# Kernel tuning notes

Measured on AMD Instinct MI355X. Metric: run time of the kernel, lower is better.

## Reference

```python
import jax, jax.numpy as jnp
import numpy as np

N = 8192      # nb_nodes
HID = 128     # hid_dim
OUT = 64      # out_dim
E = 262144    # num edges (avg degree 32)
BN_EPS = 1e-5


def setup_inputs() -> dict:
    key = jax.random.key(0)
    ks = jax.random.split(key, 10)
    x = jax.random.normal(ks[0], (N, HID), dtype=jnp.float32)
    adj = jnp.zeros((N, N), dtype=jnp.float32)  # unused by the module's forward
    src = jax.random.randint(ks[1], (E,), 0, N)
    dst = jax.random.randint(ks[2], (E,), 0, N)
    s = 0.05
    fc_w = jax.random.normal(ks[3], (HID, OUT), dtype=jnp.float32) * s
    fc_b = jnp.zeros((OUT,), dtype=jnp.float32)
    w1 = jax.random.normal(ks[4], (HID, HID), dtype=jnp.float32) * s
    w1_b = jnp.zeros((HID,), dtype=jnp.float32)
    w2 = jax.random.normal(ks[5], (HID, OUT), dtype=jnp.float32) * s
    w2_b = jnp.zeros((OUT,), dtype=jnp.float32)
    epsilon = jnp.full((N,), 0.5, dtype=jnp.float32)  # init.constant_(0.5)
    gamma = jnp.ones((OUT,), dtype=jnp.float32)
    beta = jnp.zeros((OUT,), dtype=jnp.float32)
    return {"x": x, "adj": adj, "src": src, "dst": dst,
            "fc_w": fc_w, "fc_b": fc_b, "w1": w1, "w1_b": w1_b,
            "w2": w2, "w2_b": w2_b, "epsilon": epsilon,
            "gamma": gamma, "beta": beta}


def _neighbor_sum(feat, src, dst):
    # DGL copy_src + sum: each dst node sums features of its src neighbors.
    return jax.ops.segment_sum(feat[src], dst, num_segments=N)


def reference(x, adj, src, dst, fc_w, fc_b, w1, w1_b, w2, w2_b, epsilon, gamma, beta):
    # h1 = fc(x)
    h1 = x @ fc_w + fc_b                                  # [N, OUT]
    # layer1: neighbor-sum then linear, ReLU
    h2 = jax.nn.relu(_neighbor_sum(x, src, dst) @ w1 + w1_b)   # [N, HID]
    # layer2: neighbor-sum then linear
    h2 = _neighbor_sum(h2, src, dst) @ w2 + w2_b          # [N, OUT]
    eps = epsilon[:, None]
    h = (1.0 - eps) * h1 + eps * h2                       # [N, OUT]
    ret = (h @ h.T + x @ x.T) * 0.5                       # [N, N]
    # BatchNorm1d (training mode: batch stats, biased variance)
    mean = jnp.mean(h, axis=0)
    var = jnp.var(h, axis=0)
    h_bn = (h - mean) * jax.lax.rsqrt(var + BN_EPS) * gamma + beta
    return ret, h_bn
```

## Files before the change

kernel.cpp:

```cpp
#include <hip/hip_runtime.h>
#include <hip/hip_bf16.h>

#define N_NODES 8192
#define HID 128
#define OUT_F 64
#define E_EDGES 262144
#define KTOT 192

typedef __bf16 bf16x8 __attribute__((ext_vector_type(8)));
typedef float  f32x4  __attribute__((ext_vector_type(4)));

__device__ __forceinline__ unsigned short f2bf(float f) {
    unsigned int u = __float_as_uint(f);
    u += 0x7fffu + ((u >> 16) & 1u);
    return (unsigned short)(u >> 16);
}

__global__ void count_k(const int* __restrict__ dst, int* __restrict__ cnt) {
    int e = blockIdx.x * 256 + threadIdx.x;
    if (e < E_EDGES) atomicAdd(&cnt[dst[e]], 1);
}

__global__ void scan_k(const int* __restrict__ cnt, int* __restrict__ off,
                       int* __restrict__ cursor, float* __restrict__ stats) {
    __shared__ int part[256];
    int tid = threadIdx.x;
    if (tid < 128) stats[tid] = 0.0f;
    int base = tid * 32;
    int local[32];
    int s = 0;
    #pragma unroll
    for (int j = 0; j < 32; ++j) { local[j] = s; s += cnt[base + j]; }
    part[tid] = s;
    __syncthreads();
    if (tid == 0) {
        int acc = 0;
        for (int i = 0; i < 256; ++i) { int t = part[i]; part[i] = acc; acc += t; }
    }
    __syncthreads();
    int p = part[tid];
    #pragma unroll
    for (int j = 0; j < 32; ++j) {
        int v = p + local[j];
        off[base + j] = v;
        cursor[base + j] = v;
    }
    if (tid == 255) off[N_NODES] = p + s;
}

__global__ void fill_k(const int* __restrict__ src, const int* __restrict__ dst,
                       int* __restrict__ cursor, int* __restrict__ eidx) {
    int e = blockIdx.x * 256 + threadIdx.x;
    if (e >= E_EDGES) return;
    int pos = atomicAdd(&cursor[dst[e]], 1);
    eidx[pos] = src[e];
}

__global__ __launch_bounds__(256)
void pre_k(const float* __restrict__ x,
           const float* __restrict__ fcw, const float* __restrict__ fcb,
           const float* __restrict__ w1,
           float* __restrict__ h1, float* __restrict__ y,
           unsigned short* __restrict__ G) {
    __shared__ float wS[64 * 192];
    __shared__ float xs[16 * HID];
    int tid = threadIdx.x;
    int rowbase = blockIdx.x * 16;

    for (int i = tid; i < 512; i += 256)
        *(float4*)&xs[i * 4] = *(const float4*)&x[(size_t)rowbase * HID + i * 4];

    int c = tid & 63, r0 = tid >> 6;
    float acc[3][4] = {};

    for (int kh = 0; kh < 2; ++kh) {
        __syncthreads();
        for (int i = tid; i < 1024; i += 256) {
            int k = i >> 4, qd = i & 15;
            *(float4*)&wS[k * 192 + qd * 4] =
                *(const float4*)&fcw[(size_t)(kh * 64 + k) * 64 + qd * 4];
        }
        for (int i = tid; i < 2048; i += 256) {
            int k = i >> 5, qd = i & 31;
            *(float4*)&wS[k * 192 + 64 + qd * 4] =
                *(const float4*)&w1[(size_t)(kh * 64 + k) * 128 + qd * 4];
        }
        __syncthreads();
        #pragma unroll 4
        for (int k = 0; k < 64; ++k) {
            float wa = wS[k * 192 + c];
            float wb = wS[k * 192 + 64 + c];
            float wc = wS[k * 192 + 128 + c];
            #pragma unroll
            for (int g = 0; g < 4; ++g) {
                float xv = xs[(r0 + 4 * g) * HID + kh * 64 + k];
                acc[0][g] += xv * wa;
                acc[1][g] += xv * wb;
                acc[2][g] += xv * wc;
            }
        }
    }
    float b = fcb[c];
    #pragma unroll
    for (int g = 0; g < 4; ++g) {
        int r = rowbase + r0 + 4 * g;
        h1[(size_t)r * OUT_F + c]    = acc[0][g] + b;
        y[(size_t)r * HID + c]       = acc[1][g];
        y[(size_t)r * HID + 64 + c]  = acc[2][g];
    }
    const float SC = 0.70710678f;
    for (int i = tid; i < 2048; i += 256) {
        int r = i >> 7, cc = i & 127;
        G[(size_t)(rowbase + r) * KTOT + OUT_F + cc] = f2bf(xs[r * HID + cc] * SC);
    }
}

__global__ __launch_bounds__(256)
void gather_mlp_k(const float* __restrict__ feat,
                  const int* __restrict__ eidx,
                  const int* __restrict__ off,
                  const float* __restrict__ bias,
                  const float* __restrict__ w2,
                  float* __restrict__ z) {
    __shared__ float wS[HID * 64];
    __shared__ float rowS[4][HID];
    int tid = threadIdx.x;
    int wid = tid >> 6, lane = tid & 63;

    for (int i = tid; i < 2048; i += 256)
        *(float4*)&wS[i * 4] = *(const float4*)&w2[i * 4];

    int node = blockIdx.x * 4 + wid;
    int beg = off[node], end = off[node + 1];
    float2 a0{0,0}, a1{0,0}, a2{0,0}, a3{0,0}, a4{0,0}, a5{0,0}, a6{0,0}, a7{0,0};
    int j = beg;
    for (; j + 8 <= end; j += 8) {
        int s0 = eidx[j],     s1 = eidx[j + 1], s2 = eidx[j + 2], s3 = eidx[j + 3];
        int s4 = eidx[j + 4], s5 = eidx[j + 5], s6 = eidx[j + 6], s7 = eidx[j + 7];
        float2 v0 = *((const float2*)(feat + (size_t)s0 * HID) + lane);
        float2 v1 = *((const float2*)(feat + (size_t)s1 * HID) + lane);
        float2 v2 = *((const float2*)(feat + (size_t)s2 * HID) + lane);
        float2 v3 = *((const float2*)(feat + (size_t)s3 * HID) + lane);
        float2 v4 = *((const float2*)(feat + (size_t)s4 * HID) + lane);
        float2 v5 = *((const float2*)(feat + (size_t)s5 * HID) + lane);
        float2 v6 = *((const float2*)(feat + (size_t)s6 * HID) + lane);
        float2 v7 = *((const float2*)(feat + (size_t)s7 * HID) + lane);
        a0.x += v0.x; a0.y += v0.y;  a1.x += v1.x; a1.y += v1.y;
        a2.x += v2.x; a2.y += v2.y;  a3.x += v3.x; a3.y += v3.y;
        a4.x += v4.x; a4.y += v4.y;  a5.x += v5.x; a5.y += v5.y;
        a6.x += v6.x; a6.y += v6.y;  a7.x += v7.x; a7.y += v7.y;
    }
    for (; j < end; ++j) {
        int s0 = eidx[j];
        float2 v0 = *((const float2*)(feat + (size_t)s0 * HID) + lane);
        a0.x += v0.x; a0.y += v0.y;
    }
    float2 r;
    r.x = ((a0.x + a1.x) + (a2.x + a3.x)) + ((a4.x + a5.x) + (a6.x + a7.x));
    r.y = ((a0.y + a1.y) + (a2.y + a3.y)) + ((a4.y + a5.y) + (a6.y + a7.y));
    float2 bb = *((const float2*)bias + lane);
    rowS[wid][lane * 2]     = fmaxf(r.x + bb.x, 0.0f);
    rowS[wid][lane * 2 + 1] = fmaxf(r.y + bb.y, 0.0f);
    __syncthreads();

    float acc = 0.0f;
    #pragma unroll 8
    for (int k = 0; k < HID; ++k)
        acc += rowS[wid][k] * wS[k * 64 + lane];
    z[(size_t)node * OUT_F + lane] = acc;
}

__global__ void gather_fuse_k(const float* __restrict__ z,
                              const int* __restrict__ eidx,
                              const int* __restrict__ off,
                              const float* __restrict__ h1,
                              const float* __restrict__ w2b,
                              const float* __restrict__ eps,
                              float* __restrict__ h,
                              unsigned short* __restrict__ G,
                              float* __restrict__ stats) {
    __shared__ float red[8][64];
    int tid = threadIdx.x;
    int wid = tid >> 6, lane = tid & 63;
    float s = 0.0f, q = 0.0f;
    float b = w2b[lane];
    const float SC = 0.70710678f;
    for (int t = 0; t < 4; ++t) {
        int node = blockIdx.x * 16 + wid * 4 + t;
        int beg = off[node], end = off[node + 1];
        float a0 = 0, a1 = 0, a2 = 0, a3 = 0, a4 = 0, a5 = 0, a6 = 0, a7 = 0;
        int j = beg;
        for (; j + 8 <= end; j += 8) {
            int s0 = eidx[j],     s1 = eidx[j + 1], s2 = eidx[j + 2], s3 = eidx[j + 3];
            int s4 = eidx[j + 4], s5 = eidx[j + 5], s6 = eidx[j + 6], s7 = eidx[j + 7];
            a0 += z[(size_t)s0 * OUT_F + lane];
            a1 += z[(size_t)s1 * OUT_F + lane];
            a2 += z[(size_t)s2 * OUT_F + lane];
            a3 += z[(size_t)s3 * OUT_F + lane];
            a4 += z[(size_t)s4 * OUT_F + lane];
            a5 += z[(size_t)s5 * OUT_F + lane];
            a6 += z[(size_t)s6 * OUT_F + lane];
            a7 += z[(size_t)s7 * OUT_F + lane];
        }
        for (; j < end; ++j)
            a0 += z[(size_t)eidx[j] * OUT_F + lane];
        float gs = ((a0 + a1) + (a2 + a3)) + ((a4 + a5) + (a6 + a7));
        float e = eps[node];
        float hv = (1.0f - e) * h1[(size_t)node * OUT_F + lane] + e * (gs + b);
        h[(size_t)node * OUT_F + lane] = hv;
        G[(size_t)node * KTOT + lane] = f2bf(hv * SC);
        s += hv;
        q += hv * hv;
    }
    red[wid][lane] = s;
    red[4 + wid][lane] = q;
    __syncthreads();
    if (tid < 64) {
        atomicAdd(&stats[tid],
                  (red[0][tid] + red[1][tid]) + (red[2][tid] + red[3][tid]));
    } else if (tid < 128) {
        int l = tid - 64;
        atomicAdd(&stats[64 + l],
                  (red[4][l] + red[5][l]) + (red[6][l] + red[7][l]));
    }
}

__global__ void bn_apply_k(const float* __restrict__ h,
                           const float* __restrict__ stats,
                           const float* __restrict__ gamma,
                           const float* __restrict__ beta,
                           float* __restrict__ outBN) {
    int idx = blockIdx.x * 256 + threadIdx.x;
    if (idx >= N_NODES * OUT_F) return;
    int c = idx & 63;
    const float inv_n = 1.0f / 8192.0f;
    float m = stats[c] * inv_n;
    float v = stats[64 + c] * inv_n - m * m;
    outBN[idx] = (h[idx] - m) * rsqrtf(v + 1e-5f) * gamma[c] + beta[c];
}

__global__ __launch_bounds__(256, 4)
void big_gemm_k(const unsigned short* __restrict__ G, float* __restrict__ C) {
    int bid = blockIdx.x;
    int by = (int)((sqrtf(8.0f * bid + 1.0f) - 1.0f) * 0.5f);
    while ((by + 1) * (by + 2) / 2 <= bid) ++by;
    while (by * (by + 1) / 2 > bid) --by;
    int bx = bid - by * (by + 1) / 2;

    int tid = threadIdx.x;
    int lane = tid & 63, wid = tid >> 6;
    int wm = wid >> 1, wn = wid & 1;
    int row0 = by * 128, col0 = bx * 128;

    const unsigned short* Abase =
        G + (size_t)(row0 + wm * 64 + (lane & 15)) * KTOT + (lane >> 4) * 8;
    const unsigned short* Bbase =
        G + (size_t)(col0 + wn * 64 + (lane & 15)) * KTOT + (lane >> 4) * 8;

    f32x4 acc[4][4] = {};

    #pragma unroll
    for (int kk = 0; kk < 6; ++kk) {
        bf16x8 af[4], bfr[4];
        #pragma unroll
        for (int t = 0; t < 4; ++t) {
            af[t]  = *(const bf16x8*)(Abase + (size_t)t * 16 * KTOT + kk * 32);
            bfr[t] = *(const bf16x8*)(Bbase + (size_t)t * 16 * KTOT + kk * 32);
        }
        #pragma unroll
        for (int tm = 0; tm < 4; ++tm)
            #pragma unroll
            for (int tn = 0; tn < 4; ++tn)
                acc[tm][tn] = __builtin_amdgcn_mfma_f32_16x16x32_bf16(
                    af[tm], bfr[tn], acc[tm][tn], 0, 0, 0);
    }

    int crow = row0 + wm * 64 + (lane >> 4) * 4;
    int ccol = col0 + wn * 64 + (lane & 15);
    #pragma unroll
    for (int tm = 0; tm < 4; ++tm)
        #pragma unroll
        for (int tn = 0; tn < 4; ++tn)
            #pragma unroll
            for (int r = 0; r < 4; ++r)
                __builtin_nontemporal_store(acc[tm][tn][r],
                    &C[(size_t)(crow + tm * 16 + r) * N_NODES + (ccol + tn * 16)]);

    if (bx != by) {
        int trow = col0 + wn * 64 + (lane & 15);
        int tcol = row0 + wm * 64 + (lane >> 4) * 4;
        #pragma unroll
        for (int tm = 0; tm < 4; ++tm)
            #pragma unroll
            for (int tn = 0; tn < 4; ++tn) {
                f32x4 v = acc[tm][tn];
                __builtin_nontemporal_store(v,
                    (f32x4*)&C[(size_t)(trow + tn * 16) * N_NODES + tcol + tm * 16]);
            }
    }
}

extern "C" void kernel_launch(void* const* d_in, const int* in_sizes, int n_in,
                              void* d_out, int out_size, void* d_ws, size_t ws_size,
                              hipStream_t stream) {
    const float* x    = (const float*)d_in[0];
    const int*   src  = (const int*)d_in[2];
    const int*   dst  = (const int*)d_in[3];
    const float* fcw  = (const float*)d_in[4];
    const float* fcb  = (const float*)d_in[5];
    const float* w1   = (const float*)d_in[6];
    const float* w1b  = (const float*)d_in[7];
    const float* w2   = (const float*)d_in[8];
    const float* w2b  = (const float*)d_in[9];
    const float* eps  = (const float*)d_in[10];
    const float* gamma= (const float*)d_in[11];
    const float* beta = (const float*)d_in[12];

    float* ws = (float*)d_ws;
    float* y     = ws;
    float* h1    = ws + 1048576;
    float* z     = ws + 1572864;
    float* h     = ws + 2097152;
    unsigned short* G = (unsigned short*)(ws + 2621440);
    float* stats = ws + 2621440 + 786432;
    int*   cnt    = (int*)(ws + 3408000);
    int*   off    = cnt + N_NODES;
    int*   cursor = off + N_NODES + 1;
    int*   eidx   = cursor + N_NODES;

    float* ret   = (float*)d_out;
    float* outBN = (float*)d_out + (size_t)N_NODES * N_NODES;

    hipMemsetAsync(cnt, 0, N_NODES * sizeof(int), stream);

    dim3 blk(256);

    count_k<<<E_EDGES / 256, blk, 0, stream>>>(dst, cnt);
    scan_k<<<1, blk, 0, stream>>>(cnt, off, cursor, stats);
    fill_k<<<E_EDGES / 256, blk, 0, stream>>>(src, dst, cursor, eidx);

    pre_k<<<N_NODES / 16, blk, 0, stream>>>(x, fcw, fcb, w1, h1, y, G);
    gather_mlp_k<<<N_NODES / 4, blk, 0, stream>>>(y, eidx, off, w1b, w2, z);
    gather_fuse_k<<<N_NODES / 16, blk, 0, stream>>>(z, eidx, off, h1, w2b, eps,
                                                    h, G, stats);
    bn_apply_k<<<(N_NODES * OUT_F) / 256, blk, 0, stream>>>(h, stats, gamma, beta, outBN);
    big_gemm_k<<<2080, blk, 0, stream>>>(G, ret);
}
```

Baseline: 569.9 us.

## Stage GEMM tiles in LDS and fuse BatchNorm apply into GEMM kernel

The symmetric output GEMM now cooperatively loads 128-row A and B tiles into padded shared memory in two K halves and reads MFMA fragments from LDS instead of global memory. The separate BatchNorm apply kernel is removed and its work is done by the first blocks of the GEMM launch. This aims to reduce redundant global fragment loads and one kernel launch. In exchange it adds barriers and LDS use and halves the occupancy hint, which may reduce latency hiding for the large output stores.

```diff
diff --git a/kernel.cpp b/kernel.cpp
--- a/kernel.cpp
+++ b/kernel.cpp
@@ -6,6 +6,7 @@
 #define OUT_F 64
 #define E_EDGES 262144
 #define KTOT 192
+#define LDK 104
 
 typedef __bf16 bf16x8 __attribute__((ext_vector_type(8)));
 typedef float  f32x4  __attribute__((ext_vector_type(4)));
@@ -225,54 +226,66 @@
     }
 }
 
-__global__ void bn_apply_k(const float* __restrict__ h,
-                           const float* __restrict__ stats,
-                           const float* __restrict__ gamma,
-                           const float* __restrict__ beta,
-                           float* __restrict__ outBN) {
-    int idx = blockIdx.x * 256 + threadIdx.x;
-    if (idx >= N_NODES * OUT_F) return;
-    int c = idx & 63;
-    const float inv_n = 1.0f / 8192.0f;
-    float m = stats[c] * inv_n;
-    float v = stats[64 + c] * inv_n - m * m;
-    outBN[idx] = (h[idx] - m) * rsqrtf(v + 1e-5f) * gamma[c] + beta[c];
-}
-
-__global__ __launch_bounds__(256, 4)
-void big_gemm_k(const unsigned short* __restrict__ G, float* __restrict__ C) {
+__global__ __launch_bounds__(256, 2)
+void big_gemm_k(const unsigned short* __restrict__ G, float* __restrict__ C,
+                const float* __restrict__ h, const float* __restrict__ stats,
+                const float* __restrict__ gamma, const float* __restrict__ beta,
+                float* __restrict__ outBN) {
     int bid = blockIdx.x;
+    int tid = threadIdx.x;
+
+    if (bid < 2048) {
+        int c = tid & 63, rr = tid >> 6;
+        int node = bid * 4 + rr;
+        const float inv_n = 1.0f / 8192.0f;
+        float m = stats[c] * inv_n;
+        float v = stats[64 + c] * inv_n - m * m;
+        outBN[(size_t)node * OUT_F + c] =
+            (h[(size_t)node * OUT_F + c] - m) * rsqrtf(v + 1e-5f) * gamma[c] + beta[c];
+    }
+
     int by = (int)((sqrtf(8.0f * bid + 1.0f) - 1.0f) * 0.5f);
     while ((by + 1) * (by + 2) / 2 <= bid) ++by;
     while (by * (by + 1) / 2 > bid) --by;
     int bx = bid - by * (by + 1) / 2;
 
-    int tid = threadIdx.x;
+    __shared__ unsigned short Ap[128 * LDK];
+    __shared__ unsigned short Bp[128 * LDK];
     int lane = tid & 63, wid = tid >> 6;
     int wm = wid >> 1, wn = wid & 1;
     int row0 = by * 128, col0 = bx * 128;
 
-    const unsigned short* Abase =
-        G + (size_t)(row0 + wm * 64 + (lane & 15)) * KTOT + (lane >> 4) * 8;
-    const unsigned short* Bbase =
-        G + (size_t)(col0 + wn * 64 + (lane & 15)) * KTOT + (lane >> 4) * 8;
-
     f32x4 acc[4][4] = {};
 
     #pragma unroll
-    for (int kk = 0; kk < 6; ++kk) {
-        bf16x8 af[4], bfr[4];
+    for (int kh = 0; kh < 2; ++kh) {
+        if (kh) __syncthreads();
+        for (int i = tid; i < 128 * 12; i += 256) {
+            int r = i / 12, cc = i % 12;
+            *(uint4*)(&Ap[r * LDK + cc * 8]) =
+                *(const uint4*)(G + (size_t)(row0 + r) * KTOT + kh * 96 + cc * 8);
+            *(uint4*)(&Bp[r * LDK + cc * 8]) =
+                *(const uint4*)(G + (size_t)(col0 + r) * KTOT + kh * 96 + cc * 8);
+        }
+        __syncthreads();
+        int rA = wm * 64 + (lane & 15);
+        int rB = wn * 64 + (lane & 15);
+        int klane = (lane >> 4) * 8;
         #pragma unroll
-        for (int t = 0; t < 4; ++t) {
-            af[t]  = *(const bf16x8*)(Abase + (size_t)t * 16 * KTOT + kk * 32);
-            bfr[t] = *(const bf16x8*)(Bbase + (size_t)t * 16 * KTOT + kk * 32);
-        }
-        #pragma unroll
-        for (int tm = 0; tm < 4; ++tm)
-            #pragma unroll
-            for (int tn = 0; tn < 4; ++tn)
-                acc[tm][tn] = __builtin_amdgcn_mfma_f32_16x16x32_bf16(
-                    af[tm], bfr[tn], acc[tm][tn], 0, 0, 0);
+        for (int ks = 0; ks < 3; ++ks) {
+            bf16x8 af[4], bfr[4];
+            #pragma unroll
+            for (int t = 0; t < 4; ++t) {
+                af[t]  = *(const bf16x8*)(&Ap[(rA + t * 16) * LDK + ks * 32 + klane]);
+                bfr[t] = *(const bf16x8*)(&Bp[(rB + t * 16) * LDK + ks * 32 + klane]);
+            }
+            #pragma unroll
+            for (int tm = 0; tm < 4; ++tm)
+                #pragma unroll
+                for (int tn = 0; tn < 4; ++tn)
+                    acc[tm][tn] = __builtin_amdgcn_mfma_f32_16x16x32_bf16(
+                        af[tm], bfr[tn], acc[tm][tn], 0, 0, 0);
+        }
     }
 
     int crow = row0 + wm * 64 + (lane >> 4) * 4;
@@ -343,6 +356,5 @@
     gather_mlp_k<<<N_NODES / 4, blk, 0, stream>>>(y, eidx, off, w1b, w2, z);
     gather_fuse_k<<<N_NODES / 16, blk, 0, stream>>>(z, eidx, off, h1, w2b, eps,
                                                     h, G, stats);
-    bn_apply_k<<<(N_NODES * OUT_F) / 256, blk, 0, stream>>>(h, stats, gamma, beta, outBN);
-    big_gemm_k<<<2080, blk, 0, stream>>>(G, ret);
-}
+    big_gemm_k<<<2080, blk, 0, stream>>>(G, ret, h, stats, gamma, beta, outBN);
+}
```

New measurement: 542.0 us. 4.9% less time.
